# Optimization experiments

Hardware: AMD Instinct MI355X
Metric: run time of the kernel (lower is better)

The kernel has to match this reference:

```python
import jax, jax.numpy as jnp
import numpy as np


def _lstm_scan(xs, W_ih, W_hh, b, h0, c0):
    """Run an LSTMCell over time. xs: [T, B, D]; returns (hs [T,B,H], h_T, c_T).
    PyTorch LSTMCell gate order: i, f, g, o; b = b_ih + b_hh fused."""
    H = h0.shape[-1]

    def step(carry, x_t):
        h, c = carry
        gates = x_t @ W_ih.T + h @ W_hh.T + b  # [B, 4H]
        i, f, g, o = jnp.split(gates, 4, axis=-1)
        i = jax.nn.sigmoid(i)
        f = jax.nn.sigmoid(f)
        g = jnp.tanh(g)
        o = jax.nn.sigmoid(o)
        c_new = f * c + i * g
        h_new = o * jnp.tanh(c_new)
        return (h_new, c_new), h_new

    (h_T, c_T), hs = jax.lax.scan(step, (h0, c0), xs)
    return hs, h_T, c_T


def setup_inputs() -> dict:
    key = jax.random.key(0)
    ks = jax.random.split(key, 7)
    B, T, F, H = 64, 512, 256, 1024
    s = lambda fan_in: np.sqrt(2.0) * np.sqrt(6.0 / (4 * H + fan_in))  # xavier_uniform gain=sqrt(2)
    return {
        "x": jax.random.normal(ks[0], (B, T, F), dtype=jnp.float32),
        "W_ih_e": jax.random.uniform(ks[1], (4 * H, F), jnp.float32, -s(F), s(F)),
        "W_hh_e": jax.random.uniform(ks[2], (4 * H, H), jnp.float32, -s(H), s(H)),
        "b_e": jnp.zeros((4 * H,), jnp.float32),
        "W_ih_d": jax.random.uniform(ks[3], (4 * H, H), jnp.float32, -s(H), s(H)),
        "W_hh_d": jax.random.uniform(ks[4], (4 * H, H), jnp.float32, -s(H), s(H)),
        "b_d": jnp.zeros((4 * H,), jnp.float32),
        "W_out": jax.random.uniform(ks[5], (F, H), jnp.float32, -s(F), s(F)),
        "b_out": jnp.zeros((F,), jnp.float32),
    }


def reference(x, W_ih_e, W_hh_e, b_e, W_ih_d, W_hh_d, b_d, W_out, b_out):
    B, T, F = x.shape
    H = W_hh_e.shape[1]
    xs = jnp.swapaxes(x, 0, 1)  # [T, B, F] time-major
    h0 = jnp.zeros((B, H), x.dtype)
    c0 = jnp.zeros((B, H), x.dtype)
    # Encoder: LSTMCell(F, H), collect per-step hidden states
    enc_hs, h_T, c_T = _lstm_scan(xs, W_ih_e, W_hh_e, b_e, h0, c0)  # [T, B, H]
    # Decoder: LSTMCell(H, H) over encoder hidden states, seeded with final (h, c)
    dec_hs, _, _ = _lstm_scan(enc_hs, W_ih_d, W_hh_d, b_d, h_T, c_T)  # [T, B, H]
    # Output projection H -> F
    out = jnp.einsum('tbh,fh->tbf', dec_hs, W_out) + b_out
    return jnp.swapaxes(out, 0, 1)  # [B, T, F]
```

## Files before the change

kernel.cpp:

```cpp
#include <hip/hip_runtime.h>
#include <math.h>

#define TT 512
#define BB 64
#define FF 256
#define HH 1024
#define NBLK 256
#define NCHE 5
#define NCHD 8
#define NGRP 16

typedef __attribute__((ext_vector_type(8))) short short8;
typedef __attribute__((ext_vector_type(4))) float f32x4;

__device__ __forceinline__ unsigned short f2bf(float f) {
    unsigned u = __float_as_uint(f);
    u += 0x7FFFu + ((u >> 16) & 1u);
    return (unsigned short)(u >> 16);
}
__device__ __forceinline__ float bf2f(unsigned short u) {
    return __uint_as_float((unsigned)u << 16);
}

__global__ __launch_bounds__(256) void k_cast_x(const float* __restrict__ x,
                                                unsigned short* __restrict__ xB) {
    int t = blockIdx.x;
    #pragma unroll
    for (int i = 0; i < 16; ++i) {
        int id = threadIdx.x + i * 256;
        int b  = id >> 6;
        int f4 = (id & 63) << 2;
        float4 v = *(const float4*)(x + ((size_t)b * TT + t) * FF + f4);
        ushort4 o;
        o.x = f2bf(v.x); o.y = f2bf(v.y); o.z = f2bf(v.z); o.w = f2bf(v.w);
        *(ushort4*)(xB + ((size_t)t * BB + b) * FF + f4) = o;
    }
}

__global__ __launch_bounds__(256) void k_wcast(const float* __restrict__ in,
                                               unsigned short* __restrict__ out,
                                               int n4) {
    int stride = gridDim.x * 256;
    for (int i = blockIdx.x * 256 + threadIdx.x; i < n4; i += stride) {
        float4 v = ((const float4*)in)[i];
        ushort4 o;
        o.x = f2bf(v.x); o.y = f2bf(v.y); o.z = f2bf(v.z); o.w = f2bf(v.w);
        ((ushort4*)out)[i] = o;
    }
}

__device__ __forceinline__ void gbar2(unsigned* __restrict__ bar, int phase) {
    __syncthreads();
    if (threadIdx.x == 0) {
        const unsigned GSZ = NBLK / NGRP;
        unsigned g = (unsigned)blockIdx.x & (NGRP - 1);
        __builtin_amdgcn_fence(__ATOMIC_RELEASE, "agent");
        unsigned t = __hip_atomic_fetch_add(bar + g * 32, 1u,
                                            __ATOMIC_RELAXED, __HIP_MEMORY_SCOPE_AGENT);
        if (t == (unsigned)phase * GSZ + GSZ - 1) {
            unsigned r = __hip_atomic_fetch_add(bar + NGRP * 32, 1u,
                                                __ATOMIC_RELAXED, __HIP_MEMORY_SCOPE_AGENT);
            if (r == (unsigned)phase * NGRP + NGRP - 1)
                __hip_atomic_fetch_add(bar + NGRP * 32 + 32, 1u,
                                       __ATOMIC_RELAXED, __HIP_MEMORY_SCOPE_AGENT);
        }
        while (__hip_atomic_load(bar + NGRP * 32 + 32, __ATOMIC_RELAXED,
                                 __HIP_MEMORY_SCOPE_AGENT) < (unsigned)(phase + 1))
            __builtin_amdgcn_s_sleep(2);
    }
    __syncthreads();
}

template <int NCH, int NPRE>
__device__ __forceinline__ void lstm_step(
    const short8* __restrict__ sW,
    const unsigned short* __restrict__ A1, int K1,
    const unsigned short* __restrict__ A2, int K2, int C1,
    const f32x4 bias, float& creg,
    unsigned short* __restrict__ hOut,
    unsigned* __restrict__ bar, int phase,
    int lane, int q, int u, int b)
{
    short8 av[3][8];
    auto aload = [&](short8* dst, int c) {
        const unsigned short* ap = (c < C1)
            ? A1 + (size_t)b * K1 + (size_t)c * 256
            : A2 + (size_t)b * K2 + (size_t)(c - C1) * 256;
        ap += q * 8;
        #pragma unroll
        for (int f = 0; f < 8; ++f) dst[f] = *(const short8*)(ap + f * 32);
    };

    aload(av[0], 0);
    if (NCH > 1 && NPRE > 1) aload(av[1], 1);

    if (phase >= 0) gbar2(bar, phase);

    if (NCH > 1 && NPRE <= 1) aload(av[1], 1);

    f32x4 accA = {0.f, 0.f, 0.f, 0.f};
    f32x4 accB = {0.f, 0.f, 0.f, 0.f};
    #pragma unroll
    for (int c = 0; c < NCH; ++c) {
        if (c + 2 < NCH) aload(av[(c + 2) % 3], c + 2);
        const short8* cur = av[c % 3];
        #pragma unroll
        for (int f = 0; f < 8; ++f) {
            short8 wv = sW[(c * 8 + f) * 64 + lane];
            if (f & 1) accB = __builtin_amdgcn_mfma_f32_16x16x32_bf16(wv, cur[f], accB, 0, 0, 0);
            else       accA = __builtin_amdgcn_mfma_f32_16x16x32_bf16(wv, cur[f], accA, 0, 0, 0);
        }
    }
    f32x4 acc = accA + accB;

    float pi = acc[0] + bias[0];
    float pf = acc[1] + bias[1];
    float pg = acc[2] + bias[2];
    float po = acc[3] + bias[3];
    float iv = 1.f / (1.f + __expf(-pi));
    float fv = 1.f / (1.f + __expf(-pf));
    float gv = tanhf(pg);
    float ov = 1.f / (1.f + __expf(-po));
    float cn = fv * creg + iv * gv;
    creg = cn;
    float hn = ov * tanhf(cn);
    hOut[(size_t)b * HH + u] = f2bf(hn);
}

__global__ __launch_bounds__(256, 1) void k_lstm_persist(
    const unsigned short* __restrict__ xB,
    const unsigned short* __restrict__ WihE,
    const unsigned short* __restrict__ WhhE,
    const float* __restrict__ bE,
    const unsigned short* __restrict__ WihD,
    const unsigned short* __restrict__ WhhD,
    const float* __restrict__ bD,
    unsigned short* __restrict__ encB,
    unsigned short* __restrict__ decR,
    unsigned* __restrict__ bar)
{
    __shared__ short8 sWe[NCHE * 8 * 64];
    __shared__ short8 sWd[NCHD * 8 * 64];

    const int tid  = threadIdx.x;
    const int lane = tid & 63;
    const int w    = tid >> 6;
    const int q    = lane >> 4;
    const int n    = lane & 15;
    const int j0   = blockIdx.x * 4;
    const int rrow = (n & 3) * HH + j0 + (n >> 2);
    const size_t SB = (size_t)BB * HH;

    #pragma unroll
    for (int i = 0; i < 2 * NCHE; ++i) {
        int g = i * 4 + w;
        int c = g >> 3, f = g & 7;
        const unsigned short* Wp; int Ks; int cl;
        if (c < 1) { Wp = WihE; Ks = FF; cl = c; }
        else       { Wp = WhhE; Ks = HH; cl = c - 1; }
        sWe[g * 64 + lane] =
            *(const short8*)(Wp + (size_t)rrow * Ks + (size_t)cl * 256 + f * 32 + q * 8);
    }
    #pragma unroll
    for (int i = 0; i < 2 * NCHD; ++i) {
        int g = i * 4 + w;
        int c = g >> 3, f = g & 7;
        const unsigned short* Wp; int cl;
        if (c < 4) { Wp = WihD; cl = c; }
        else       { Wp = WhhD; cl = c - 4; }
        sWd[g * 64 + lane] =
            *(const short8*)(Wp + (size_t)rrow * HH + (size_t)cl * 256 + f * 32 + q * 8);
    }
    __syncthreads();

    const int u = j0 + q;
    const int b = w * 16 + n;
    const f32x4 biasE = {bE[u], bE[HH + u], bE[2 * HH + u], bE[3 * HH + u]};
    const f32x4 biasD = {bD[u], bD[HH + u], bD[2 * HH + u], bD[3 * HH + u]};

    float creg = 0.f;

    lstm_step<1, 1>(sWe, xB, FF, xB, FF, 1, biasE, creg,
                    encB, bar, -1, lane, q, u, b);
    for (int t = 1; t < TT; ++t) {
        lstm_step<NCHE, 1>(sWe, xB + (size_t)t * BB * FF, FF,
                           encB + (size_t)(t - 1) * SB, HH, 1,
                           biasE, creg, encB + (size_t)t * SB,
                           bar, t - 1, lane, q, u, b);
    }

    for (int t = 0; t < TT; ++t) {
        const unsigned short* A2 = (t == 0) ? encB + (size_t)(TT - 1) * SB
                                            : decR + (size_t)(t - 1) * SB;
        lstm_step<NCHD, 2>(sWd, encB + (size_t)t * SB, HH, A2, HH, 4,
                           biasD, creg, decR + (size_t)t * SB,
                           bar, (TT - 1) + t, lane, q, u, b);
    }
}

__global__ __launch_bounds__(256) void k_out_proj_r(
    const unsigned short* __restrict__ decR,
    const float* __restrict__ Wout,
    const float* __restrict__ bout,
    float* __restrict__ out)
{
    int t  = blockIdx.x;
    int fg = blockIdx.y;
    const int lane = threadIdx.x & 63;
    const int wv   = __builtin_amdgcn_readfirstlane(threadIdx.x >> 6);
    const int f0   = fg * 64 + wv * 16;
    const unsigned short* a = decR + ((size_t)t * BB + lane) * HH;

    float acc[16];
    #pragma unroll
    for (int i = 0; i < 16; ++i) acc[i] = bout[f0 + i];

    for (int k8 = 0; k8 < HH / 8; ++k8) {
        short8 hv8 = *(const short8*)(a + k8 * 8);
        #pragma unroll
        for (int uu = 0; uu < 8; ++uu) {
            float hv = bf2f((unsigned short)hv8[uu]);
            #pragma unroll
            for (int i = 0; i < 16; ++i)
                acc[i] = fmaf(Wout[(size_t)(f0 + i) * HH + k8 * 8 + uu], hv, acc[i]);
        }
    }

    float* op = out + ((size_t)lane * TT + t) * FF + f0;
    #pragma unroll
    for (int i = 0; i < 16; i += 4) {
        float4 v = make_float4(acc[i], acc[i + 1], acc[i + 2], acc[i + 3]);
        *(float4*)(op + i) = v;
    }
}

template <int NCH>
__global__ __launch_bounds__(256) void k_step_lds(
    const unsigned short* __restrict__ A1, const unsigned short* __restrict__ W1, int K1,
    const unsigned short* __restrict__ A2, const unsigned short* __restrict__ W2, int K2,
    int C1,
    const float* __restrict__ bias,
    float* __restrict__ Cbuf,
    unsigned short* __restrict__ hOut,
    float* __restrict__ chunkOut)
{
    __shared__ short8 sW[NCH * 8 * 64];

    const int tid  = threadIdx.x;
    const int lane = tid & 63;
    const int w    = tid >> 6;
    const int q    = lane >> 4;
    const int n    = lane & 15;
    const int j0   = blockIdx.x * 4;
    const int rrow = (n & 3) * HH + j0 + (n >> 2);

    short8 av[3][8];

    auto aload = [&](short8* dst, int c) {
        const unsigned short* ap = (c < C1)
            ? A1 + (size_t)(w * 16 + n) * K1 + (size_t)c * 256
            : A2 + (size_t)(w * 16 + n) * K2 + (size_t)(c - C1) * 256;
        ap += q * 8;
        #pragma unroll
        for (int f = 0; f < 8; ++f) dst[f] = *(const short8*)(ap + f * 32);
    };

    aload(av[0], 0);
    if (NCH > 1) aload(av[1], 1);

    #pragma unroll
    for (int i = 0; i < 2 * NCH; ++i) {
        int g = i * 4 + w;
        int c = g >> 3, f = g & 7;
        const unsigned short* Wp; int Ks; int cl;
        if (c < C1) { Wp = W1; Ks = K1; cl = c; }
        else        { Wp = W2; Ks = K2; cl = c - C1; }
        sW[g * 64 + lane] =
            *(const short8*)(Wp + (size_t)rrow * Ks + (size_t)cl * 256 + f * 32 + q * 8);
    }
    __syncthreads();

    f32x4 accA = {0.f, 0.f, 0.f, 0.f};
    f32x4 accB = {0.f, 0.f, 0.f, 0.f};
    #pragma unroll
    for (int c = 0; c < NCH; ++c) {
        if (c + 2 < NCH) aload(av[(c + 2) % 3], c + 2);
        const short8* cur = av[c % 3];
        #pragma unroll
        for (int f = 0; f < 8; ++f) {
            short8 wv = sW[(c * 8 + f) * 64 + lane];
            if (f & 1) accB = __builtin_amdgcn_mfma_f32_16x16x32_bf16(wv, cur[f], accB, 0, 0, 0);
            else       accA = __builtin_amdgcn_mfma_f32_16x16x32_bf16(wv, cur[f], accA, 0, 0, 0);
        }
    }
    f32x4 acc = accA + accB;

    const int u = j0 + q;
    const int b = w * 16 + n;
    float pi = acc[0] + bias[u];
    float pf = acc[1] + bias[HH + u];
    float pg = acc[2] + bias[2 * HH + u];
    float po = acc[3] + bias[3 * HH + u];
    float iv = 1.f / (1.f + __expf(-pi));
    float fv = 1.f / (1.f + __expf(-pf));
    float gv = tanhf(pg);
    float ov = 1.f / (1.f + __expf(-po));
    size_t cix = (size_t)u * BB + b;
    float c  = Cbuf[cix];
    float cn = fv * c + iv * gv;
    Cbuf[cix] = cn;
    float hn = ov * tanhf(cn);
    hOut[(size_t)b * HH + u] = f2bf(hn);
    if (chunkOut) chunkOut[cix] = hn;
}

__device__ __forceinline__ void seg_f32(const unsigned short* __restrict__ ap0,
                                        const float* __restrict__ wp0,
                                        int nch, f32x4& acc) {
    const unsigned short* ap = ap0;
    const float* wp = wp0;
    #pragma unroll 2
    for (int c = 0; c < nch; ++c) {
        float4 wa = *(const float4*)wp;
        float4 wb = *(const float4*)(wp + 4);
        short8 av = *(const short8*)ap;
        short8 wv;
        wv[0] = (short)f2bf(wa.x); wv[1] = (short)f2bf(wa.y);
        wv[2] = (short)f2bf(wa.z); wv[3] = (short)f2bf(wa.w);
        wv[4] = (short)f2bf(wb.x); wv[5] = (short)f2bf(wb.y);
        wv[6] = (short)f2bf(wb.z); wv[7] = (short)f2bf(wb.w);
        acc = __builtin_amdgcn_mfma_f32_16x16x32_bf16(wv, av, acc, 0, 0, 0);
        ap += 32; wp += 32;
    }
}

__global__ __launch_bounds__(256) void k_step_f32w(
    const unsigned short* __restrict__ A1, const float* __restrict__ W1, int K1,
    const unsigned short* __restrict__ A2, const float* __restrict__ W2, int K2,
    const float* __restrict__ bias,
    float* __restrict__ Cbuf, unsigned short* __restrict__ hOut,
    float* __restrict__ chunkOut)
{
    const int tid  = threadIdx.x;
    const int lane = tid & 63;
    const int w    = tid >> 6;
    const int q    = lane >> 4;
    const int n    = lane & 15;
    const int j0   = blockIdx.x * 4;
    const int rrow = (n & 3) * HH + j0 + (n >> 2);

    f32x4 acc = {0.f, 0.f, 0.f, 0.f};
    seg_f32(A1 + (size_t)(w * 16 + n) * K1 + q * 8,
            W1 + (size_t)rrow * K1 + q * 8, K1 >> 5, acc);
    if (K2)
        seg_f32(A2 + (size_t)(w * 16 + n) * HH + q * 8,
                W2 + (size_t)rrow * HH + q * 8, HH >> 5, acc);

    const int u = j0 + q;
    const int b = w * 16 + n;
    float pi = acc[0] + bias[u];
    float pf = acc[1] + bias[HH + u];
    float pg = acc[2] + bias[2 * HH + u];
    float po = acc[3] + bias[3 * HH + u];
    float iv = 1.f / (1.f + __expf(-pi));
    float fv = 1.f / (1.f + __expf(-pf));
    float gv = tanhf(pg);
    float ov = 1.f / (1.f + __expf(-po));
    size_t cix = (size_t)u * BB + b;
    float c  = Cbuf[cix];
    float cn = fv * c + iv * gv;
    Cbuf[cix] = cn;
    float hn = ov * tanhf(cn);
    hOut[(size_t)b * HH + u] = f2bf(hn);
    if (chunkOut) chunkOut[cix] = hn;
}

__global__ __launch_bounds__(256) void k_out_proj(
    const float* __restrict__ chunk,
    const float* __restrict__ Wout,
    const float* __restrict__ bout,
    float* __restrict__ out,
    int t0)
{
    int tl = blockIdx.x;
    int t  = t0 + tl;
    int fg = blockIdx.y;
    const int lane = threadIdx.x & 63;
    const int wv   = __builtin_amdgcn_readfirstlane(threadIdx.x >> 6);
    const int f0   = fg * 64 + wv * 16;
    const float* a = chunk + (size_t)tl * HH * BB;

    float acc[16];
    #pragma unroll
    for (int i = 0; i < 16; ++i) acc[i] = bout[f0 + i];

    for (int k = 0; k < HH; k += 4) {
        #pragma unroll
        for (int u = 0; u < 4; ++u) {
            float hv = a[(size_t)(k + u) * BB + lane];
            #pragma unroll
            for (int i = 0; i < 16; ++i)
                acc[i] = fmaf(Wout[(size_t)(f0 + i) * HH + k + u], hv, acc[i]);
        }
    }

    float* op = out + ((size_t)lane * TT + t) * FF + f0;
    #pragma unroll
    for (int i = 0; i < 16; i += 4) {
        float4 v = make_float4(acc[i], acc[i + 1], acc[i + 2], acc[i + 3]);
        *(float4*)(op + i) = v;
    }
}

extern "C" void kernel_launch(void* const* d_in, const int* in_sizes, int n_in,
                              void* d_out, int out_size, void* d_ws, size_t ws_size,
                              hipStream_t stream) {
    const float* x     = (const float*)d_in[0];
    const float* Wih_e = (const float*)d_in[1];
    const float* Whh_e = (const float*)d_in[2];
    const float* b_e   = (const float*)d_in[3];
    const float* Wih_d = (const float*)d_in[4];
    const float* Whh_d = (const float*)d_in[5];
    const float* b_d   = (const float*)d_in[6];
    const float* Wout  = (const float*)d_in[7];
    const float* bout  = (const float*)d_in[8];
    float* out = (float*)d_out;

    const size_t SB = (size_t)BB * HH;

    unsigned short* xB = (unsigned short*)d_out;

    {
        char* p = (char*)d_ws;
        unsigned* bar = (unsigned*)p; p += 4096;
        unsigned short* encB  = (unsigned short*)p; p += (size_t)TT * SB * 2;
        unsigned short* decR  = (unsigned short*)p; p += (size_t)TT * SB * 2;
        unsigned short* WihEb = (unsigned short*)p; p += (size_t)4 * HH * FF * 2;
        unsigned short* WhhEb = (unsigned short*)p; p += (size_t)4 * HH * HH * 2;
        unsigned short* WihDb = (unsigned short*)p; p += (size_t)4 * HH * HH * 2;
        unsigned short* WhhDb = (unsigned short*)p; p += (size_t)4 * HH * HH * 2;
        size_t need = (size_t)(p - (char*)d_ws);

        if (ws_size >= need) {
            hipMemsetAsync(bar, 0, 4096, stream);
            k_cast_x<<<TT, 256, 0, stream>>>(x, xB);
            k_wcast<<<1024, 256, 0, stream>>>(Wih_e, WihEb, 4 * HH * FF / 4);
            k_wcast<<<1024, 256, 0, stream>>>(Whh_e, WhhEb, 4 * HH * HH / 4);
            k_wcast<<<1024, 256, 0, stream>>>(Wih_d, WihDb, 4 * HH * HH / 4);
            k_wcast<<<1024, 256, 0, stream>>>(Whh_d, WhhDb, 4 * HH * HH / 4);

            void* args[] = {
                (void*)&xB, (void*)&WihEb, (void*)&WhhEb, (void*)&b_e,
                (void*)&WihDb, (void*)&WhhDb, (void*)&b_d,
                (void*)&encB, (void*)&decR, (void*)&bar};
            hipLaunchCooperativeKernel((const void*)k_lstm_persist,
                                       dim3(NBLK), dim3(256), args, 0, stream);

            k_out_proj_r<<<dim3(TT, 4), 256, 0, stream>>>(decR, Wout, bout, out);
            return;
        }
    }

    char* p = (char*)d_ws;
    unsigned short* encB  = (unsigned short*)p; p += (size_t)TT * SB * 2;
    unsigned short* dech0 = (unsigned short*)p; p += SB * 2;
    unsigned short* dech1 = (unsigned short*)p; p += SB * 2;
    float* cbuf = (float*)p; p += SB * 4;
    size_t used  = (size_t)(p - (char*)d_ws);
    size_t avail = ws_size > used ? ws_size - used : 0;

    const size_t WE_B = ((size_t)4 * HH * FF + (size_t)4 * HH * HH) * 2;
    const size_t WD_B = ((size_t)4 * HH * HH) * 2 * 2;
    const size_t CH8  = (size_t)8 * SB * 4;

    bool wbAll = (avail >= WE_B + WD_B + CH8);
    bool wbEnc = wbAll || (avail >= WE_B + CH8);

    unsigned short *WihEb = 0, *WhhEb = 0, *WihDb = 0, *WhhDb = 0;
    if (wbEnc) {
        WihEb = (unsigned short*)p; p += (size_t)4 * HH * FF * 2;
        WhhEb = (unsigned short*)p; p += (size_t)4 * HH * HH * 2;
        avail -= WE_B;
    }
    if (wbAll) {
        WihDb = (unsigned short*)p; p += (size_t)4 * HH * HH * 2;
        WhhDb = (unsigned short*)p; p += (size_t)4 * HH * HH * 2;
        avail -= WD_B;
    }
    int C = 8;
    if      (avail >= (size_t)64 * SB * 4) C = 64;
    else if (avail >= (size_t)32 * SB * 4) C = 32;
    else if (avail >= (size_t)16 * SB * 4) C = 16;
    float* chunk = (float*)p;

    hipMemsetAsync(cbuf, 0, SB * 4, stream);
    k_cast_x<<<TT, 256, 0, stream>>>(x, xB);
    if (wbEnc) {
        k_wcast<<<1024, 256, 0, stream>>>(Wih_e, WihEb, 4 * HH * FF / 4);
        k_wcast<<<1024, 256, 0, stream>>>(Whh_e, WhhEb, 4 * HH * HH / 4);
    }
    if (wbAll) {
        k_wcast<<<1024, 256, 0, stream>>>(Wih_d, WihDb, 4 * HH * HH / 4);
        k_wcast<<<1024, 256, 0, stream>>>(Whh_d, WhhDb, 4 * HH * HH / 4);
    }

    for (int t = 0; t < TT; ++t) {
        const unsigned short* A1 = xB + (size_t)t * BB * FF;
        const unsigned short* A2 = t ? encB + (size_t)(t - 1) * SB : (unsigned short*)0;
        unsigned short* hOut = encB + (size_t)t * SB;
        if (wbEnc) {
            if (t == 0)
                k_step_lds<1><<<256, 256, 0, stream>>>(A1, WihEb, FF, A2, WhhEb, HH,
                                                       1, b_e, cbuf, hOut, (float*)0);
            else
                k_step_lds<5><<<256, 256, 0, stream>>>(A1, WihEb, FF, A2, WhhEb, HH,
                                                       1, b_e, cbuf, hOut, (float*)0);
        } else {
            k_step_f32w<<<256, 256, 0, stream>>>(A1, Wih_e, FF, A2, Whh_e,
                                                 t ? HH : 0, b_e, cbuf, hOut, (float*)0);
        }
    }

    for (int t = 0; t < TT; ++t) {
        const unsigned short* A1 = encB + (size_t)t * SB;
        const unsigned short* A2 = (t == 0) ? encB + (size_t)(TT - 1) * SB
                                            : ((t & 1) ? dech1 : dech0);
        unsigned short* hOut = ((t + 1) & 1) ? dech1 : dech0;
        int l = t & (C - 1);
        float* ch = chunk + (size_t)l * SB;
        if (wbAll)
            k_step_lds<8><<<256, 256, 0, stream>>>(A1, WihDb, HH, A2, WhhDb, HH,
                                                   4, b_d, cbuf, hOut, ch);
        else
            k_step_f32w<<<256, 256, 0, stream>>>(A1, Wih_d, FF, A2, Whh_d, HH,
                                                 b_d, cbuf, hOut, ch);
        if (l == C - 1)
            k_out_proj<<<dim3(C, 4), 256, 0, stream>>>(chunk, Wout, bout, out,
                                                       t - (C - 1));
    }
}
```

Measured before the change: 10.59 ms.

## Replace hierarchical grid barrier with per-wave flag publish and polling

Swaps the two-level atomic grid barrier for per-wave progress flags. Each wave publishes its timestep once its hidden-state store has drained, and every wave polls all 1024 flags with 64-bit atomic loads before reading the next step's inputs. Hidden outputs are packed via shuffles into one 64-bit atomic store per row of four units, replacing scattered 16-bit stores. This removes __syncthreads and the serialized atomic chain from each step, but every wave now polls many flags, and memory ordering rests on relaxed atomics plus an explicit vmcnt wait.

After: 12.05 ms. 13.7% more time.

```diff
diff --git a/kernel.cpp b/kernel.cpp
--- a/kernel.cpp
+++ b/kernel.cpp
@@ -8,7 +8,6 @@
 #define NBLK 256
 #define NCHE 5
 #define NCHD 8
-#define NGRP 16
 
 typedef __attribute__((ext_vector_type(8))) short short8;
 typedef __attribute__((ext_vector_type(4))) float f32x4;
@@ -49,26 +48,30 @@
     }
 }
 
-__device__ __forceinline__ void gbar2(unsigned* __restrict__ bar, int phase) {
-    __syncthreads();
-    if (threadIdx.x == 0) {
-        const unsigned GSZ = NBLK / NGRP;
-        unsigned g = (unsigned)blockIdx.x & (NGRP - 1);
-        __builtin_amdgcn_fence(__ATOMIC_RELEASE, "agent");
-        unsigned t = __hip_atomic_fetch_add(bar + g * 32, 1u,
-                                            __ATOMIC_RELAXED, __HIP_MEMORY_SCOPE_AGENT);
-        if (t == (unsigned)phase * GSZ + GSZ - 1) {
-            unsigned r = __hip_atomic_fetch_add(bar + NGRP * 32, 1u,
-                                                __ATOMIC_RELAXED, __HIP_MEMORY_SCOPE_AGENT);
-            if (r == (unsigned)phase * NGRP + NGRP - 1)
-                __hip_atomic_fetch_add(bar + NGRP * 32 + 32, 1u,
-                                       __ATOMIC_RELAXED, __HIP_MEMORY_SCOPE_AGENT);
-        }
-        while (__hip_atomic_load(bar + NGRP * 32 + 32, __ATOMIC_RELAXED,
-                                 __HIP_MEMORY_SCOPE_AGENT) < (unsigned)(phase + 1))
-            __builtin_amdgcn_s_sleep(2);
-    }
-    __syncthreads();
+__device__ __forceinline__ void publish(unsigned* __restrict__ flags,
+                                        int widx, unsigned val) {
+    asm volatile("s_waitcnt vmcnt(0)" ::: "memory");
+    if ((threadIdx.x & 63) == 0)
+        __hip_atomic_store(flags + widx, val, __ATOMIC_RELAXED,
+                           __HIP_MEMORY_SCOPE_AGENT);
+}
+
+__device__ __forceinline__ void waitall(const unsigned* __restrict__ flags,
+                                        int lane, unsigned tgt) {
+    const unsigned long long* f2 = (const unsigned long long*)flags;
+    for (;;) {
+        bool ok = true;
+        #pragma unroll
+        for (int k = 0; k < 8; ++k) {
+            unsigned long long v = __hip_atomic_load(f2 + lane + 64 * k,
+                                                     __ATOMIC_RELAXED,
+                                                     __HIP_MEMORY_SCOPE_AGENT);
+            ok &= ((unsigned)v >= tgt) && ((unsigned)(v >> 32) >= tgt);
+        }
+        if (__all(ok)) break;
+        __builtin_amdgcn_s_sleep(2);
+    }
+    asm volatile("" ::: "memory");
 }
 
 template <int NCH, int NPRE>
@@ -78,8 +81,8 @@
     const unsigned short* __restrict__ A2, int K2, int C1,
     const f32x4 bias, float& creg,
     unsigned short* __restrict__ hOut,
-    unsigned* __restrict__ bar, int phase,
-    int lane, int q, int u, int b)
+    unsigned* __restrict__ flags, int tgt, int widx, unsigned pub,
+    int lane, int q, int n, int j0, int u, int b)
 {
     short8 av[3][8];
     auto aload = [&](short8* dst, int c) {
@@ -94,7 +97,7 @@
     aload(av[0], 0);
     if (NCH > 1 && NPRE > 1) aload(av[1], 1);
 
-    if (phase >= 0) gbar2(bar, phase);
+    if (tgt > 0) waitall(flags, lane, (unsigned)tgt);
 
     if (NCH > 1 && NPRE <= 1) aload(av[1], 1);
 
@@ -124,7 +127,19 @@
     float cn = fv * creg + iv * gv;
     creg = cn;
     float hn = ov * tanhf(cn);
-    hOut[(size_t)b * HH + u] = f2bf(hn);
+
+    unsigned hv = (unsigned)f2bf(hn);
+    unsigned v0 = (unsigned)__shfl((int)hv, n);
+    unsigned v1 = (unsigned)__shfl((int)hv, n + 16);
+    unsigned v2 = (unsigned)__shfl((int)hv, n + 32);
+    unsigned v3 = (unsigned)__shfl((int)hv, n + 48);
+    if (q == 0) {
+        unsigned long long pk = (unsigned long long)(v0 | (v1 << 16)) |
+                                ((unsigned long long)(v2 | (v3 << 16)) << 32);
+        __hip_atomic_store((unsigned long long*)(hOut + (size_t)b * HH + j0), pk,
+                           __ATOMIC_RELAXED, __HIP_MEMORY_SCOPE_AGENT);
+    }
+    if (pub) publish(flags, widx, pub);
 }
 
 __global__ __launch_bounds__(256, 1) void k_lstm_persist(
@@ -137,7 +152,7 @@
     const float* __restrict__ bD,
     unsigned short* __restrict__ encB,
     unsigned short* __restrict__ decR,
-    unsigned* __restrict__ bar)
+    unsigned* __restrict__ flags)
 {
     __shared__ short8 sWe[NCHE * 8 * 64];
     __shared__ short8 sWd[NCHD * 8 * 64];
@@ -150,6 +165,7 @@
     const int j0   = blockIdx.x * 4;
     const int rrow = (n & 3) * HH + j0 + (n >> 2);
     const size_t SB = (size_t)BB * HH;
+    const int widx = blockIdx.x * 4 + w;
 
     #pragma unroll
     for (int i = 0; i < 2 * NCHE; ++i) {
@@ -181,20 +197,23 @@
     float creg = 0.f;
 
     lstm_step<1, 1>(sWe, xB, FF, xB, FF, 1, biasE, creg,
-                    encB, bar, -1, lane, q, u, b);
+                    encB, flags, 0, widx, 1u, lane, q, n, j0, u, b);
     for (int t = 1; t < TT; ++t) {
         lstm_step<NCHE, 1>(sWe, xB + (size_t)t * BB * FF, FF,
                            encB + (size_t)(t - 1) * SB, HH, 1,
                            biasE, creg, encB + (size_t)t * SB,
-                           bar, t - 1, lane, q, u, b);
+                           flags, t, widx, (unsigned)(t + 1),
+                           lane, q, n, j0, u, b);
     }
 
     for (int t = 0; t < TT; ++t) {
         const unsigned short* A2 = (t == 0) ? encB + (size_t)(TT - 1) * SB
                                             : decR + (size_t)(t - 1) * SB;
+        unsigned pub = (t == TT - 1) ? 0u : (unsigned)(TT + t + 1);
         lstm_step<NCHD, 2>(sWd, encB + (size_t)t * SB, HH, A2, HH, 4,
                            biasD, creg, decR + (size_t)t * SB,
-                           bar, (TT - 1) + t, lane, q, u, b);
+                           flags, TT + t, widx, pub,
+                           lane, q, n, j0, u, b);
     }
 }
 
@@ -432,7 +451,7 @@
 
     {
         char* p = (char*)d_ws;
-        unsigned* bar = (unsigned*)p; p += 4096;
+        unsigned* flags = (unsigned*)p; p += 4096;
         unsigned short* encB  = (unsigned short*)p; p += (size_t)TT * SB * 2;
         unsigned short* decR  = (unsigned short*)p; p += (size_t)TT * SB * 2;
         unsigned short* WihEb = (unsigned short*)p; p += (size_t)4 * HH * FF * 2;
@@ -442,7 +461,7 @@
         size_t need = (size_t)(p - (char*)d_ws);
 
         if (ws_size >= need) {
-            hipMemsetAsync(bar, 0, 4096, stream);
+            hipMemsetAsync(flags, 0, 4096, stream);
             k_cast_x<<<TT, 256, 0, stream>>>(x, xB);
             k_wcast<<<1024, 256, 0, stream>>>(Wih_e, WihEb, 4 * HH * FF / 4);
             k_wcast<<<1024, 256, 0, stream>>>(Whh_e, WhhEb, 4 * HH * HH / 4);
@@ -452,7 +471,7 @@
             void* args[] = {
                 (void*)&xB, (void*)&WihEb, (void*)&WhhEb, (void*)&b_e,
                 (void*)&WihDb, (void*)&WhhDb, (void*)&b_d,
-                (void*)&encB, (void*)&decR, (void*)&bar};
+                (void*)&encB, (void*)&decR, (void*)&flags};
             hipLaunchCooperativeKernel((const void*)k_lstm_persist,
                                        dim3(NBLK), dim3(256), args, 0, stream);
 
```
